# Performance work log

Hardware: AMD Instinct MI355X
Metric: run time of the kernel (lower is better)

Reference implementation:

```python
import jax, jax.numpy as jnp
import numpy as np

NUM_CODES = 512
CODE_DIM = 64
COMMITMENT_COST = 0.1
DECAY = 0.9
EPS = 1e-5


def setup_inputs() -> dict:
    key = jax.random.key(0)
    k1, k2, k3 = jax.random.split(key, 3)
    B, L, D, K = 32, 4096, CODE_DIM, NUM_CODES
    z_e = jax.random.normal(k1, (B, L, D), dtype=jnp.float32)
    emb = jax.random.uniform(k2, (K, D), dtype=jnp.float32, minval=-1.0 / K, maxval=1.0 / K)
    ema_cluster_size = jnp.ones((K,), dtype=jnp.float32)
    ema_w = emb + 0.01 * jax.random.normal(k3, (K, D), dtype=jnp.float32)
    return {"z_e": z_e, "emb": emb, "ema_cluster_size": ema_cluster_size, "ema_w": ema_w}


def reference(z_e, emb, ema_cluster_size, ema_w):
    B, L, D = z_e.shape
    K = emb.shape[0]
    flat = z_e.reshape(-1, D)                                   # [N, D]
    dists = (jnp.sum(flat * flat, axis=1, keepdims=True)
             - 2.0 * flat @ emb.T
             + jnp.sum(emb * emb, axis=1)[None, :])
    codes = jnp.argmin(dists, axis=1)                           # [N] int
    z_q = emb[codes].reshape(B, L, D)
    # straight-through estimator
    z_q_st = z_e + jax.lax.stop_gradient(z_q - z_e)
    # EMA updates (training, no_grad) via direct scatter-reduce instead of one-hot matmul
    cluster_size = jax.ops.segment_sum(jnp.ones_like(codes, dtype=z_e.dtype), codes, num_segments=K)
    new_ecs = ema_cluster_size * DECAY + cluster_size * (1.0 - DECAY)
    dw = jax.ops.segment_sum(flat, codes, num_segments=K)       # [K, D]
    new_ema_w = ema_w * DECAY + dw * (1.0 - DECAY)
    n = jnp.sum(new_ecs)
    cs_smoothed = (new_ecs + EPS) / (n + K * EPS) * n
    new_emb = new_ema_w / (cs_smoothed[:, None] + EPS)
    # commitment loss (z_q detached)
    commit = jnp.mean((z_e - jax.lax.stop_gradient(z_q)) ** 2)
    loss_vq = COMMITMENT_COST * commit
    return (z_q_st, loss_vq, codes.reshape(B, L), new_ecs, new_ema_w, new_emb)
```

## Files before the change

### kernel.cpp

```cpp
#include <hip/hip_runtime.h>
#include <math.h>

#define NROWS 131072
#define DIM 64
#define NCODE 512

#define OUT_ZQ    0
#define OUT_LOSS  8388608
#define OUT_CODES 8388609
#define OUT_ECS   8519681
#define OUT_EMAW  8520193
#define OUT_EMB   8552961

#define WS_LOSS    0
#define WS_N       8
#define WS_COUNTS  16
#define WS_OFFSETS 2064
#define WS_CURSOR  4112
#define WS_CSUM    6160
#define WS_CODESI  8208
#define WS_DW4     8208
#define WS_BUCKET  532496
#define WS_BYTES   1056784
#define WS_ZERO_BYTES 2064

#define DECAY_C ((float)0.9)
#define OMD_C   ((float)(1.0 - 0.9))
#define EPS_C   ((float)1e-5)

#define R4(M, b)  M(b) M((b) + 1) M((b) + 2) M((b) + 3)
#define R16(M, b) R4(M, b) R4(M, (b) + 4) R4(M, (b) + 8) R4(M, (b) + 12)

__device__ __forceinline__ float np_pairwise64_sq(const float* v) {
    float r[8];
#pragma unroll
    for (int j = 0; j < 8; ++j) r[j] = __fmul_rn(v[j], v[j]);
#pragma unroll
    for (int b = 1; b < 8; ++b) {
#pragma unroll
        for (int j = 0; j < 8; ++j)
            r[j] = __fadd_rn(r[j], __fmul_rn(v[8 * b + j], v[8 * b + j]));
    }
    return __fadd_rn(__fadd_rn(__fadd_rn(r[0], r[1]), __fadd_rn(r[2], r[3])),
                     __fadd_rn(__fadd_rn(r[4], r[5]), __fadd_rn(r[6], r[7])));
}

__global__ void k_csum(const float* __restrict__ emb, float* __restrict__ csum) {
    int k = blockIdx.x * blockDim.x + threadIdx.x;
    if (k >= NCODE) return;
    float e[DIM];
#pragma unroll
    for (int d = 0; d < DIM; d += 4) {
        float4 v = *reinterpret_cast<const float4*>(emb + (size_t)k * DIM + d);
        e[d] = v.x; e[d + 1] = v.y; e[d + 2] = v.z; e[d + 3] = v.w;
    }
    csum[k] = np_pairwise64_sq(e);
}

__global__ __launch_bounds__(256) void k_scores(
        const float* __restrict__ ze, const float* __restrict__ emb,
        const float* __restrict__ csum, float* __restrict__ out,
        int* __restrict__ codes_i, int* __restrict__ counts,
        double* __restrict__ lossAcc) {
    __shared__ float xs[DIM][128];
    __shared__ float ms[128];
    __shared__ int   hi_i[128];
    __shared__ int h[NCODE];
    __shared__ double ls[4];
    int t = threadIdx.x;
    int c = t & 127;
    int half = t >> 7;
    for (int i = t; i < NCODE; i += 256) h[i] = 0;

    int row = blockIdx.x * 128 + c;
    const float* x = ze + (size_t)row * DIM;

    float r0, r1, r2, r3, r4, r5, r6, r7;
    {
        float4 va = *reinterpret_cast<const float4*>(x + 0);
        float4 vb = *reinterpret_cast<const float4*>(x + 4);
        float d0 = __fadd_rn(va.x, va.x), d1 = __fadd_rn(va.y, va.y);
        float d2 = __fadd_rn(va.z, va.z), d3 = __fadd_rn(va.w, va.w);
        float d4 = __fadd_rn(vb.x, vb.x), d5 = __fadd_rn(vb.y, vb.y);
        float d6 = __fadd_rn(vb.z, vb.z), d7 = __fadd_rn(vb.w, vb.w);
        xs[0][c] = d0; xs[1][c] = d1; xs[2][c] = d2; xs[3][c] = d3;
        xs[4][c] = d4; xs[5][c] = d5; xs[6][c] = d6; xs[7][c] = d7;
        r0 = __fmul_rn(d0, d0); r1 = __fmul_rn(d1, d1);
        r2 = __fmul_rn(d2, d2); r3 = __fmul_rn(d3, d3);
        r4 = __fmul_rn(d4, d4); r5 = __fmul_rn(d5, d5);
        r6 = __fmul_rn(d6, d6); r7 = __fmul_rn(d7, d7);
    }
#define LD8(b) { \
        float4 va = *reinterpret_cast<const float4*>(x + 8 * (b)); \
        float4 vb = *reinterpret_cast<const float4*>(x + 8 * (b) + 4); \
        float d0 = __fadd_rn(va.x, va.x), d1 = __fadd_rn(va.y, va.y); \
        float d2 = __fadd_rn(va.z, va.z), d3 = __fadd_rn(va.w, va.w); \
        float d4 = __fadd_rn(vb.x, vb.x), d5 = __fadd_rn(vb.y, vb.y); \
        float d6 = __fadd_rn(vb.z, vb.z), d7 = __fadd_rn(vb.w, vb.w); \
        xs[8 * (b) + 0][c] = d0; xs[8 * (b) + 1][c] = d1; \
        xs[8 * (b) + 2][c] = d2; xs[8 * (b) + 3][c] = d3; \
        xs[8 * (b) + 4][c] = d4; xs[8 * (b) + 5][c] = d5; \
        xs[8 * (b) + 6][c] = d6; xs[8 * (b) + 7][c] = d7; \
        r0 = __fadd_rn(r0, __fmul_rn(d0, d0)); r1 = __fadd_rn(r1, __fmul_rn(d1, d1)); \
        r2 = __fadd_rn(r2, __fmul_rn(d2, d2)); r3 = __fadd_rn(r3, __fmul_rn(d3, d3)); \
        r4 = __fadd_rn(r4, __fmul_rn(d4, d4)); r5 = __fadd_rn(r5, __fmul_rn(d5, d5)); \
        r6 = __fadd_rn(r6, __fmul_rn(d6, d6)); r7 = __fadd_rn(r7, __fmul_rn(d7, d7)); }
    LD8(1) LD8(2) LD8(3) LD8(4) LD8(5) LD8(6) LD8(7)
    float A = __fmul_rn(0.25f,
        __fadd_rn(__fadd_rn(__fadd_rn(r0, r1), __fadd_rn(r2, r3)),
                  __fadd_rn(__fadd_rn(r4, r5), __fadd_rn(r6, r7))));

    int kbase = __builtin_amdgcn_readfirstlane(half << 8);

    float m1 = 3.4e38f;
    int i1 = kbase;
#define FMAD(dd) { const float xv = xs[dd][c]; \
        a0 = __builtin_fmaf(xv, e[(dd)      ], a0); \
        a1 = __builtin_fmaf(xv, e[(dd) +  64], a1); \
        a2 = __builtin_fmaf(xv, e[(dd) + 128], a2); \
        a3 = __builtin_fmaf(xv, e[(dd) + 192], a3); \
        a4 = __builtin_fmaf(xv, e[(dd) + 256], a4); \
        a5 = __builtin_fmaf(xv, e[(dd) + 320], a5); \
        a6 = __builtin_fmaf(xv, e[(dd) + 384], a6); \
        a7 = __builtin_fmaf(xv, e[(dd) + 448], a7); }
    for (int kk = 0; kk < NCODE / 2; kk += 8) {
        int k = kbase + kk;
        const float* e = emb + (size_t)k * DIM;
        float a0 = 0.f, a1 = 0.f, a2 = 0.f, a3 = 0.f;
        float a4 = 0.f, a5 = 0.f, a6 = 0.f, a7 = 0.f;
        R16(FMAD, 0) R16(FMAD, 16) R16(FMAD, 32) R16(FMAD, 48)
        float t0 = __fadd_rn(__fsub_rn(A, a0), csum[k + 0]);
        float t1 = __fadd_rn(__fsub_rn(A, a1), csum[k + 1]);
        float t2 = __fadd_rn(__fsub_rn(A, a2), csum[k + 2]);
        float t3 = __fadd_rn(__fsub_rn(A, a3), csum[k + 3]);
        float t4 = __fadd_rn(__fsub_rn(A, a4), csum[k + 4]);
        float t5 = __fadd_rn(__fsub_rn(A, a5), csum[k + 5]);
        float t6 = __fadd_rn(__fsub_rn(A, a6), csum[k + 6]);
        float t7 = __fadd_rn(__fsub_rn(A, a7), csum[k + 7]);
        if (t0 < m1) { m1 = t0; i1 = k; }
        if (t1 < m1) { m1 = t1; i1 = k + 1; }
        if (t2 < m1) { m1 = t2; i1 = k + 2; }
        if (t3 < m1) { m1 = t3; i1 = k + 3; }
        if (t4 < m1) { m1 = t4; i1 = k + 4; }
        if (t5 < m1) { m1 = t5; i1 = k + 5; }
        if (t6 < m1) { m1 = t6; i1 = k + 6; }
        if (t7 < m1) { m1 = t7; i1 = k + 7; }
    }
    if (half) { ms[c] = m1; hi_i[c] = i1; }
    __syncthreads();

    double lsum = 0.0;
    if (!half) {
        float mh = ms[c];
        int ih = hi_i[c];
        if (mh < m1) { m1 = mh; i1 = ih; }
        out[OUT_CODES + row] = (float)i1;
        codes_i[row] = i1;
        atomicAdd(&h[i1], 1);

        const float* e1 = emb + (size_t)i1 * DIM;
        float* zq = out + OUT_ZQ + (size_t)row * DIM;
#define ZQ4(q) { \
        float4 ev = *reinterpret_cast<const float4*>(e1 + 4 * (q)); \
        float xa = __fmul_rn(0.5f, xs[4 * (q) + 0][c]); \
        float xb = __fmul_rn(0.5f, xs[4 * (q) + 1][c]); \
        float xc = __fmul_rn(0.5f, xs[4 * (q) + 2][c]); \
        float xd = __fmul_rn(0.5f, xs[4 * (q) + 3][c]); \
        float ta = __fsub_rn(ev.x, xa); \
        float tb = __fsub_rn(ev.y, xb); \
        float tc = __fsub_rn(ev.z, xc); \
        float td = __fsub_rn(ev.w, xd); \
        float4 o; \
        o.x = __fadd_rn(xa, ta); \
        o.y = __fadd_rn(xb, tb); \
        o.z = __fadd_rn(xc, tc); \
        o.w = __fadd_rn(xd, td); \
        *reinterpret_cast<float4*>(zq + 4 * (q)) = o; \
        lsum += (double)ta * ta + (double)tb * tb + (double)tc * tc + (double)td * td; }
        R16(ZQ4, 0)
    }

    for (int off = 32; off; off >>= 1) lsum += __shfl_down(lsum, off);
    int wid = t >> 6;
    if ((t & 63) == 0) ls[wid] = lsum;
    __syncthreads();
    if (t == 0) atomicAdd(lossAcc, (ls[0] + ls[1]) + (ls[2] + ls[3]));
    for (int k = t; k < NCODE; k += 256) {
        int cc = h[k];
        if (cc) atomicAdd(&counts[k], cc);
    }
}

__global__ __launch_bounds__(512) void k_scan(
        const int* __restrict__ counts, int* __restrict__ offsets, int* __restrict__ cursor,
        const float* __restrict__ ecs_in, float* __restrict__ out, float* __restrict__ n_out) {
    __shared__ int sa[NCODE], sb[NCODE];
    __shared__ float red[NCODE];
    int k = threadIdx.x;
    int c = counts[k];
    sa[k] = c;
    float v = __fadd_rn(__fmul_rn(ecs_in[k], DECAY_C), __fmul_rn((float)c, OMD_C));
    out[OUT_ECS + k] = v;
    red[k] = v;
    __syncthreads();
    int* src = sa;
    int* dst = sb;
    for (int off = 1; off < NCODE; off <<= 1) {
        dst[k] = (k >= off) ? src[k - off] + src[k] : src[k];
        __syncthreads();
        int* tp = src; src = dst; dst = tp;
    }
    offsets[k] = src[k] - c;
    cursor[k]  = src[k] - c;
    for (int s = NCODE / 2; s > 0; s >>= 1) {
        if (k < s) red[k] += red[k + s];
        __syncthreads();
    }
    if (k == 0) n_out[0] = red[0];
}

__global__ __launch_bounds__(256) void k_scatter(
        const int* __restrict__ codes_i, int* __restrict__ cursor, int* __restrict__ bucket) {
    int row = blockIdx.x * 256 + threadIdx.x;
    int c = codes_i[row];
    int pos = atomicAdd(&cursor[c], 1);
    bucket[pos] = row;
}

__global__ __launch_bounds__(256) void k_dw(
        const float* __restrict__ ze, const int* __restrict__ bucket,
        const int* __restrict__ offsets, const int* __restrict__ counts,
        float* __restrict__ dw4) {
    __shared__ float p[4][DIM];
    int k = blockIdx.x >> 2;
    int q = blockIdx.x & 3;
    int w = threadIdx.x >> 6;
    int d = threadIdx.x & 63;
    int s = offsets[k];
    int n = counts[k];
    float acc0 = 0.f, acc1 = 0.f;
    int i = q + 4 * w;
    for (; i + 16 < n; i += 32) {
        int ra = bucket[s + i];
        int rb = bucket[s + i + 16];
        acc0 += ze[(size_t)ra * DIM + d];
        acc1 += ze[(size_t)rb * DIM + d];
    }
    if (i < n) acc0 += ze[(size_t)bucket[s + i] * DIM + d];
    p[w][d] = acc0 + acc1;
    __syncthreads();
    if (w == 0) dw4[((size_t)q * NCODE + k) * DIM + d] = (p[0][d] + p[1][d]) + (p[2][d] + p[3][d]);
}

__global__ __launch_bounds__(256) void k_final(
        const float* __restrict__ ema_w, const float* __restrict__ dw4,
        const float* __restrict__ n_ptr, const double* __restrict__ lossAcc,
        float* __restrict__ out) {
    int i = blockIdx.x * blockDim.x + threadIdx.x;
    if (i >= NCODE * DIM) return;
    int k = i >> 6;
    float dsum = __fadd_rn(__fadd_rn(dw4[i], dw4[i + NCODE * DIM]),
                           __fadd_rn(dw4[i + 2 * NCODE * DIM], dw4[i + 3 * NCODE * DIM]));
    float w = __fadd_rn(__fmul_rn(ema_w[i], DECAY_C), __fmul_rn(dsum, OMD_C));
    out[OUT_EMAW + i] = w;
    float n = n_ptr[0];
    float necs = out[OUT_ECS + k];
    float cs = (necs + EPS_C) / (n + (float)NCODE * EPS_C) * n;
    out[OUT_EMB + i] = w / (cs + EPS_C);
    if (i == 0) out[OUT_LOSS] = (float)(0.1 * (lossAcc[0] / (double)((size_t)NROWS * DIM)));
}

extern "C" void kernel_launch(void* const* d_in, const int* in_sizes, int n_in,
                              void* d_out, int out_size, void* d_ws, size_t ws_size,
                              hipStream_t stream) {
    const float* ze   = (const float*)d_in[0];
    const float* emb  = (const float*)d_in[1];
    const float* ecs  = (const float*)d_in[2];
    const float* emaw = (const float*)d_in[3];
    float* out = (float*)d_out;
    char* ws = (char*)d_ws;
    double* lossAcc = (double*)(ws + WS_LOSS);
    float*  n_out   = (float*)(ws + WS_N);
    int*    counts  = (int*)(ws + WS_COUNTS);
    int*    offsets = (int*)(ws + WS_OFFSETS);
    int*    cursor  = (int*)(ws + WS_CURSOR);
    float*  csum    = (float*)(ws + WS_CSUM);
    int*    codes_i = (int*)(ws + WS_CODESI);
    float*  dw4     = (float*)(ws + WS_DW4);
    int*    bucket  = (int*)(ws + WS_BUCKET);

    hipMemsetAsync(d_ws, 0, WS_ZERO_BYTES, stream);
    hipLaunchKernelGGL(k_csum, dim3(2), dim3(256), 0, stream, emb, csum);
    hipLaunchKernelGGL(k_scores, dim3(NROWS / 128), dim3(256), 0, stream,
                       ze, emb, csum, out, codes_i, counts, lossAcc);
    hipLaunchKernelGGL(k_scan, dim3(1), dim3(512), 0, stream,
                       counts, offsets, cursor, ecs, out, n_out);
    hipLaunchKernelGGL(k_scatter, dim3(NROWS / 256), dim3(256), 0, stream,
                       codes_i, cursor, bucket);
    hipLaunchKernelGGL(k_dw, dim3(NCODE * 4), dim3(256), 0, stream,
                       ze, bucket, offsets, counts, dw4);
    hipLaunchKernelGGL(k_final, dim3(NCODE * DIM / 256), dim3(256), 0, stream,
                       emaw, dw4, n_out, lossAcc, out);
}
```

Baseline: 241.2 us.

## Compute distances with split-bf16 MFMA and rescue near-tie rows in fp32

```diff
diff --git a/kernel.cpp b/kernel.cpp
--- a/kernel.cpp
+++ b/kernel.cpp
@@ -4,6 +4,8 @@
 #define NROWS 131072
 #define DIM 64
 #define NCODE 512
+#define FLAG_CAP 32768
+#define THR 6e-5f
 
 #define OUT_ZQ    0
 #define OUT_LOSS  8388608
@@ -14,22 +16,32 @@
 
 #define WS_LOSS    0
 #define WS_N       8
+#define WS_FLAGC   12
 #define WS_COUNTS  16
 #define WS_OFFSETS 2064
 #define WS_CURSOR  4112
 #define WS_CSUM    6160
-#define WS_CODESI  8208
-#define WS_DW4     8208
-#define WS_BUCKET  532496
-#define WS_BYTES   1056784
+#define WS_EHI     8208
+#define WS_ELO     73744
+#define WS_CODESI  139280
+#define WS_DW4     139280
+#define WS_BUCKET  663568
+#define WS_FLAGR   663568
+#define WS_BYTES   1187856
 #define WS_ZERO_BYTES 2064
 
 #define DECAY_C ((float)0.9)
 #define OMD_C   ((float)(1.0 - 0.9))
 #define EPS_C   ((float)1e-5)
 
-#define R4(M, b)  M(b) M((b) + 1) M((b) + 2) M((b) + 3)
-#define R16(M, b) R4(M, b) R4(M, (b) + 4) R4(M, (b) + 8) R4(M, (b) + 12)
+typedef float f32x4 __attribute__((ext_vector_type(4)));
+typedef short short8v __attribute__((ext_vector_type(8)));
+
+__device__ __forceinline__ unsigned short bf16_rne_bits(float f) {
+    unsigned int u = __float_as_uint(f);
+    unsigned int r = u + 0x7fffu + ((u >> 16) & 1u);
+    return (unsigned short)(r >> 16);
+}
 
 __device__ __forceinline__ float np_pairwise64_sq(const float* v) {
     float r[8];
@@ -57,129 +69,204 @@
     csum[k] = np_pairwise64_sq(e);
 }
 
-__global__ __launch_bounds__(256) void k_scores(
+__global__ __launch_bounds__(256) void k_split(
+        const float* __restrict__ emb, unsigned short* __restrict__ ehi,
+        unsigned short* __restrict__ elo) {
+    int i = blockIdx.x * 256 + threadIdx.x;
+    if (i >= NCODE * DIM) return;
+    float v = emb[i];
+    unsigned short h = bf16_rne_bits(v);
+    float hf = __uint_as_float((unsigned int)h << 16);
+    ehi[i] = h;
+    elo[i] = bf16_rne_bits(v - hf);
+}
+
+#define CVTE(H, L, j, val) { \
+    unsigned int ub = __float_as_uint(val); \
+    unsigned int rr = ub + 0x7fffu + ((ub >> 16) & 1u); \
+    unsigned short hb = (unsigned short)(rr >> 16); \
+    float hf2 = __uint_as_float(((unsigned int)hb) << 16); \
+    float lof = (val) - hf2; \
+    unsigned int ul = __float_as_uint(lof); \
+    unsigned int rl = ul + 0x7fffu + ((ul >> 16) & 1u); \
+    H[j] = (short)hb; L[j] = (short)(rl >> 16); }
+
+__global__ __launch_bounds__(256, 1) void k_mfma(
+        const float* __restrict__ ze, const unsigned short* __restrict__ ehi,
+        const unsigned short* __restrict__ elo, const float* __restrict__ csum,
+        float* __restrict__ out, int* __restrict__ codes_i,
+        int* __restrict__ flagC, int* __restrict__ flagR) {
+    __shared__ float cs[NCODE];
+    for (int i = threadIdx.x; i < NCODE; i += 256) cs[i] = csum[i];
+    __syncthreads();
+    int wid = threadIdx.x >> 6;
+    int lane = threadIdx.x & 63;
+    int r16 = lane & 15;
+    int kg = lane >> 4;
+    int rowbase = blockIdx.x * 128 + wid * 32;
+
+    short8v ahi[2][2], alo[2][2];
+#define LOADA(rt, hf) { \
+        const float4* ap = reinterpret_cast<const float4*>( \
+            ze + (size_t)(rowbase + (rt) * 16 + r16) * DIM + (hf) * 32 + 8 * kg); \
+        float4 u = ap[0], w = ap[1]; \
+        CVTE(ahi[rt][hf], alo[rt][hf], 0, u.x) CVTE(ahi[rt][hf], alo[rt][hf], 1, u.y) \
+        CVTE(ahi[rt][hf], alo[rt][hf], 2, u.z) CVTE(ahi[rt][hf], alo[rt][hf], 3, u.w) \
+        CVTE(ahi[rt][hf], alo[rt][hf], 4, w.x) CVTE(ahi[rt][hf], alo[rt][hf], 5, w.y) \
+        CVTE(ahi[rt][hf], alo[rt][hf], 6, w.z) CVTE(ahi[rt][hf], alo[rt][hf], 7, w.w) }
+    LOADA(0, 0) LOADA(0, 1) LOADA(1, 0) LOADA(1, 1)
+
+    float m1v[2][4], m2v[2][4];
+    int i1v[2][4];
+#pragma unroll
+    for (int rt = 0; rt < 2; ++rt)
+#pragma unroll
+        for (int j = 0; j < 4; ++j) { m1v[rt][j] = 3.4e38f; m2v[rt][j] = 3.4e38f; i1v[rt][j] = 0; }
+
+#define UPD(C, rt, reg) { \
+        float s = __builtin_fmaf(-2.f, C[reg], csv); \
+        if (s < m1v[rt][reg]) { m2v[rt][reg] = m1v[rt][reg]; m1v[rt][reg] = s; i1v[rt][reg] = codeIdx; } \
+        else if (s < m2v[rt][reg]) { m2v[rt][reg] = s; } }
+
+    for (int t = 0; t < 32; ++t) {
+        const short8v* bh = reinterpret_cast<const short8v*>(
+            ehi + (size_t)(t * 16 + r16) * DIM + 8 * kg);
+        const short8v* bl = reinterpret_cast<const short8v*>(
+            elo + (size_t)(t * 16 + r16) * DIM + 8 * kg);
+        short8v bh0 = bh[0], bh1 = bh[4];
+        short8v bl0 = bl[0], bl1 = bl[4];
+        f32x4 c0 = {0.f, 0.f, 0.f, 0.f};
+        f32x4 c1 = {0.f, 0.f, 0.f, 0.f};
+        c0 = __builtin_amdgcn_mfma_f32_16x16x32_bf16(ahi[0][0], bh0, c0, 0, 0, 0);
+        c0 = __builtin_amdgcn_mfma_f32_16x16x32_bf16(ahi[0][1], bh1, c0, 0, 0, 0);
+        c0 = __builtin_amdgcn_mfma_f32_16x16x32_bf16(alo[0][0], bh0, c0, 0, 0, 0);
+        c0 = __builtin_amdgcn_mfma_f32_16x16x32_bf16(alo[0][1], bh1, c0, 0, 0, 0);
+        c0 = __builtin_amdgcn_mfma_f32_16x16x32_bf16(ahi[0][0], bl0, c0, 0, 0, 0);
+        c0 = __builtin_amdgcn_mfma_f32_16x16x32_bf16(ahi[0][1], bl1, c0, 0, 0, 0);
+        c1 = __builtin_amdgcn_mfma_f32_16x16x32_bf16(ahi[1][0], bh0, c1, 0, 0, 0);
+        c1 = __builtin_amdgcn_mfma_f32_16x16x32_bf16(ahi[1][1], bh1, c1, 0, 0, 0);
+        c1 = __builtin_amdgcn_mfma_f32_16x16x32_bf16(alo[1][0], bh0, c1, 0, 0, 0);
+        c1 = __builtin_amdgcn_mfma_f32_16x16x32_bf16(alo[1][1], bh1, c1, 0, 0, 0);
+        c1 = __builtin_amdgcn_mfma_f32_16x16x32_bf16(ahi[1][0], bl0, c1, 0, 0, 0);
+        c1 = __builtin_amdgcn_mfma_f32_16x16x32_bf16(ahi[1][1], bl1, c1, 0, 0, 0);
+        float csv = cs[t * 16 + r16];
+        int codeIdx = t * 16 + r16;
+        UPD(c0, 0, 0) UPD(c0, 0, 1) UPD(c0, 0, 2) UPD(c0, 0, 3)
+        UPD(c1, 1, 0) UPD(c1, 1, 1) UPD(c1, 1, 2) UPD(c1, 1, 3)
+    }
+
+#define RED(rt, reg, mask) { \
+        float om1 = __shfl_xor(m1v[rt][reg], mask); \
+        int   oi  = __shfl_xor(i1v[rt][reg], mask); \
+        float om2 = __shfl_xor(m2v[rt][reg], mask); \
+        if (om1 < m1v[rt][reg]) { \
+            m2v[rt][reg] = fminf(m1v[rt][reg], om2); m1v[rt][reg] = om1; i1v[rt][reg] = oi; \
+        } else if (om1 > m1v[rt][reg]) { \
+            m2v[rt][reg] = fminf(m2v[rt][reg], om1); \
+        } else { \
+            if (oi < i1v[rt][reg]) i1v[rt][reg] = oi; \
+            m2v[rt][reg] = m1v[rt][reg]; } }
+#define RED4(rt, reg) RED(rt, reg, 1) RED(rt, reg, 2) RED(rt, reg, 4) RED(rt, reg, 8)
+    RED4(0, 0) RED4(0, 1) RED4(0, 2) RED4(0, 3)
+    RED4(1, 0) RED4(1, 1) RED4(1, 2) RED4(1, 3)
+
+    if (r16 == 0) {
+        int g = lane >> 4;
+#define WOUT(rt, reg) { \
+        int row = rowbase + (rt) * 16 + 4 * g + (reg); \
+        out[OUT_CODES + row] = (float)i1v[rt][reg]; \
+        codes_i[row] = i1v[rt][reg]; \
+        if (m2v[rt][reg] - m1v[rt][reg] < THR) { \
+            int pos = atomicAdd(flagC, 1); \
+            if (pos < FLAG_CAP) flagR[pos] = row; } }
+        WOUT(0, 0) WOUT(0, 1) WOUT(0, 2) WOUT(0, 3)
+        WOUT(1, 0) WOUT(1, 1) WOUT(1, 2) WOUT(1, 3)
+    }
+}
+
+__global__ __launch_bounds__(64) void k_rescue(
         const float* __restrict__ ze, const float* __restrict__ emb,
         const float* __restrict__ csum, float* __restrict__ out,
-        int* __restrict__ codes_i, int* __restrict__ counts,
-        double* __restrict__ lossAcc) {
-    __shared__ float xs[DIM][128];
-    __shared__ float ms[128];
-    __shared__ int   hi_i[128];
+        int* __restrict__ codes_i, const int* __restrict__ flagC,
+        const int* __restrict__ flagR) {
+    __shared__ float x2s[DIM];
+    int nf = *flagC;
+    if (nf > FLAG_CAP) nf = FLAG_CAP;
+    int lane = threadIdx.x;
+    for (int i = blockIdx.x; i < nf; i += gridDim.x) {
+        int row = flagR[i];
+        __syncthreads();
+        float v = ze[(size_t)row * DIM + lane];
+        x2s[lane] = __fadd_rn(v, v);
+        __syncthreads();
+        float r[8];
+#pragma unroll
+        for (int j = 0; j < 8; ++j) r[j] = __fmul_rn(x2s[j], x2s[j]);
+#pragma unroll
+        for (int b = 1; b < 8; ++b) {
+#pragma unroll
+            for (int j = 0; j < 8; ++j)
+                r[j] = __fadd_rn(r[j], __fmul_rn(x2s[8 * b + j], x2s[8 * b + j]));
+        }
+        float A = __fmul_rn(0.25f,
+            __fadd_rn(__fadd_rn(__fadd_rn(r[0], r[1]), __fadd_rn(r[2], r[3])),
+                      __fadd_rn(__fadd_rn(r[4], r[5]), __fadd_rn(r[6], r[7]))));
+        float m1 = 3.4e38f;
+        int i1 = 0x7fffffff;
+#pragma unroll
+        for (int kk = 0; kk < 8; ++kk) {
+            int k = lane * 8 + kk;
+            const float* e = emb + (size_t)k * DIM;
+            float a = 0.f;
+#pragma unroll
+            for (int d = 0; d < DIM; ++d) a = __builtin_fmaf(x2s[d], e[d], a);
+            float t = __fadd_rn(__fsub_rn(A, a), csum[k]);
+            if (t < m1) { m1 = t; i1 = k; }
+        }
+        for (int off = 32; off; off >>= 1) {
+            float ov = __shfl_xor(m1, off);
+            int oi = __shfl_xor(i1, off);
+            if (ov < m1 || (ov == m1 && oi < i1)) { m1 = ov; i1 = oi; }
+        }
+        if (lane == 0) {
+            out[OUT_CODES + row] = (float)i1;
+            codes_i[row] = i1;
+        }
+    }
+}
+
+__global__ __launch_bounds__(256) void k_apply(
+        const float* __restrict__ ze, const float* __restrict__ emb,
+        const int* __restrict__ codes_i, float* __restrict__ out,
+        int* __restrict__ counts, double* __restrict__ lossAcc) {
     __shared__ int h[NCODE];
     __shared__ double ls[4];
     int t = threadIdx.x;
-    int c = t & 127;
-    int half = t >> 7;
     for (int i = t; i < NCODE; i += 256) h[i] = 0;
-
-    int row = blockIdx.x * 128 + c;
+    __syncthreads();
+    int row = blockIdx.x * 256 + t;
+    int code = codes_i[row];
+    atomicAdd(&h[code], 1);
     const float* x = ze + (size_t)row * DIM;
-
-    float r0, r1, r2, r3, r4, r5, r6, r7;
-    {
-        float4 va = *reinterpret_cast<const float4*>(x + 0);
-        float4 vb = *reinterpret_cast<const float4*>(x + 4);
-        float d0 = __fadd_rn(va.x, va.x), d1 = __fadd_rn(va.y, va.y);
-        float d2 = __fadd_rn(va.z, va.z), d3 = __fadd_rn(va.w, va.w);
-        float d4 = __fadd_rn(vb.x, vb.x), d5 = __fadd_rn(vb.y, vb.y);
-        float d6 = __fadd_rn(vb.z, vb.z), d7 = __fadd_rn(vb.w, vb.w);
-        xs[0][c] = d0; xs[1][c] = d1; xs[2][c] = d2; xs[3][c] = d3;
-        xs[4][c] = d4; xs[5][c] = d5; xs[6][c] = d6; xs[7][c] = d7;
-        r0 = __fmul_rn(d0, d0); r1 = __fmul_rn(d1, d1);
-        r2 = __fmul_rn(d2, d2); r3 = __fmul_rn(d3, d3);
-        r4 = __fmul_rn(d4, d4); r5 = __fmul_rn(d5, d5);
-        r6 = __fmul_rn(d6, d6); r7 = __fmul_rn(d7, d7);
-    }
-#define LD8(b) { \
-        float4 va = *reinterpret_cast<const float4*>(x + 8 * (b)); \
-        float4 vb = *reinterpret_cast<const float4*>(x + 8 * (b) + 4); \
-        float d0 = __fadd_rn(va.x, va.x), d1 = __fadd_rn(va.y, va.y); \
-        float d2 = __fadd_rn(va.z, va.z), d3 = __fadd_rn(va.w, va.w); \
-        float d4 = __fadd_rn(vb.x, vb.x), d5 = __fadd_rn(vb.y, vb.y); \
-        float d6 = __fadd_rn(vb.z, vb.z), d7 = __fadd_rn(vb.w, vb.w); \
-        xs[8 * (b) + 0][c] = d0; xs[8 * (b) + 1][c] = d1; \
-        xs[8 * (b) + 2][c] = d2; xs[8 * (b) + 3][c] = d3; \
-        xs[8 * (b) + 4][c] = d4; xs[8 * (b) + 5][c] = d5; \
-        xs[8 * (b) + 6][c] = d6; xs[8 * (b) + 7][c] = d7; \
-        r0 = __fadd_rn(r0, __fmul_rn(d0, d0)); r1 = __fadd_rn(r1, __fmul_rn(d1, d1)); \
-        r2 = __fadd_rn(r2, __fmul_rn(d2, d2)); r3 = __fadd_rn(r3, __fmul_rn(d3, d3)); \
-        r4 = __fadd_rn(r4, __fmul_rn(d4, d4)); r5 = __fadd_rn(r5, __fmul_rn(d5, d5)); \
-        r6 = __fadd_rn(r6, __fmul_rn(d6, d6)); r7 = __fadd_rn(r7, __fmul_rn(d7, d7)); }
-    LD8(1) LD8(2) LD8(3) LD8(4) LD8(5) LD8(6) LD8(7)
-    float A = __fmul_rn(0.25f,
-        __fadd_rn(__fadd_rn(__fadd_rn(r0, r1), __fadd_rn(r2, r3)),
-                  __fadd_rn(__fadd_rn(r4, r5), __fadd_rn(r6, r7))));
-
-    int kbase = __builtin_amdgcn_readfirstlane(half << 8);
-
-    float m1 = 3.4e38f;
-    int i1 = kbase;
-#define FMAD(dd) { const float xv = xs[dd][c]; \
-        a0 = __builtin_fmaf(xv, e[(dd)      ], a0); \
-        a1 = __builtin_fmaf(xv, e[(dd) +  64], a1); \
-        a2 = __builtin_fmaf(xv, e[(dd) + 128], a2); \
-        a3 = __builtin_fmaf(xv, e[(dd) + 192], a3); \
-        a4 = __builtin_fmaf(xv, e[(dd) + 256], a4); \
-        a5 = __builtin_fmaf(xv, e[(dd) + 320], a5); \
-        a6 = __builtin_fmaf(xv, e[(dd) + 384], a6); \
-        a7 = __builtin_fmaf(xv, e[(dd) + 448], a7); }
-    for (int kk = 0; kk < NCODE / 2; kk += 8) {
-        int k = kbase + kk;
-        const float* e = emb + (size_t)k * DIM;
-        float a0 = 0.f, a1 = 0.f, a2 = 0.f, a3 = 0.f;
-        float a4 = 0.f, a5 = 0.f, a6 = 0.f, a7 = 0.f;
-        R16(FMAD, 0) R16(FMAD, 16) R16(FMAD, 32) R16(FMAD, 48)
-        float t0 = __fadd_rn(__fsub_rn(A, a0), csum[k + 0]);
-        float t1 = __fadd_rn(__fsub_rn(A, a1), csum[k + 1]);
-        float t2 = __fadd_rn(__fsub_rn(A, a2), csum[k + 2]);
-        float t3 = __fadd_rn(__fsub_rn(A, a3), csum[k + 3]);
-        float t4 = __fadd_rn(__fsub_rn(A, a4), csum[k + 4]);
-        float t5 = __fadd_rn(__fsub_rn(A, a5), csum[k + 5]);
-        float t6 = __fadd_rn(__fsub_rn(A, a6), csum[k + 6]);
-        float t7 = __fadd_rn(__fsub_rn(A, a7), csum[k + 7]);
-        if (t0 < m1) { m1 = t0; i1 = k; }
-        if (t1 < m1) { m1 = t1; i1 = k + 1; }
-        if (t2 < m1) { m1 = t2; i1 = k + 2; }
-        if (t3 < m1) { m1 = t3; i1 = k + 3; }
-        if (t4 < m1) { m1 = t4; i1 = k + 4; }
-        if (t5 < m1) { m1 = t5; i1 = k + 5; }
-        if (t6 < m1) { m1 = t6; i1 = k + 6; }
-        if (t7 < m1) { m1 = t7; i1 = k + 7; }
-    }
-    if (half) { ms[c] = m1; hi_i[c] = i1; }
-    __syncthreads();
-
+    const float* e = emb + (size_t)code * DIM;
+    float* zq = out + OUT_ZQ + (size_t)row * DIM;
     double lsum = 0.0;
-    if (!half) {
-        float mh = ms[c];
-        int ih = hi_i[c];
-        if (mh < m1) { m1 = mh; i1 = ih; }
-        out[OUT_CODES + row] = (float)i1;
-        codes_i[row] = i1;
-        atomicAdd(&h[i1], 1);
-
-        const float* e1 = emb + (size_t)i1 * DIM;
-        float* zq = out + OUT_ZQ + (size_t)row * DIM;
-#define ZQ4(q) { \
-        float4 ev = *reinterpret_cast<const float4*>(e1 + 4 * (q)); \
-        float xa = __fmul_rn(0.5f, xs[4 * (q) + 0][c]); \
-        float xb = __fmul_rn(0.5f, xs[4 * (q) + 1][c]); \
-        float xc = __fmul_rn(0.5f, xs[4 * (q) + 2][c]); \
-        float xd = __fmul_rn(0.5f, xs[4 * (q) + 3][c]); \
-        float ta = __fsub_rn(ev.x, xa); \
-        float tb = __fsub_rn(ev.y, xb); \
-        float tc = __fsub_rn(ev.z, xc); \
-        float td = __fsub_rn(ev.w, xd); \
-        float4 o; \
-        o.x = __fadd_rn(xa, ta); \
-        o.y = __fadd_rn(xb, tb); \
-        o.z = __fadd_rn(xc, tc); \
-        o.w = __fadd_rn(xd, td); \
-        *reinterpret_cast<float4*>(zq + 4 * (q)) = o; \
-        lsum += (double)ta * ta + (double)tb * tb + (double)tc * tc + (double)td * td; }
-        R16(ZQ4, 0)
-    }
-
+#pragma unroll
+    for (int d = 0; d < DIM; d += 4) {
+        float4 xv = *reinterpret_cast<const float4*>(x + d);
+        float4 ev = *reinterpret_cast<const float4*>(e + d);
+        float ta = __fsub_rn(ev.x, xv.x);
+        float tb = __fsub_rn(ev.y, xv.y);
+        float tc = __fsub_rn(ev.z, xv.z);
+        float td = __fsub_rn(ev.w, xv.w);
+        float4 o;
+        o.x = __fadd_rn(xv.x, ta);
+        o.y = __fadd_rn(xv.y, tb);
+        o.z = __fadd_rn(xv.z, tc);
+        o.w = __fadd_rn(xv.w, td);
+        *reinterpret_cast<float4*>(zq + d) = o;
+        lsum += (double)ta * ta + (double)tb * tb + (double)tc * tc + (double)td * td;
+    }
     for (int off = 32; off; off >>= 1) lsum += __shfl_down(lsum, off);
     int wid = t >> 6;
     if ((t & 63) == 0) ls[wid] = lsum;
@@ -281,18 +368,27 @@
     char* ws = (char*)d_ws;
     double* lossAcc = (double*)(ws + WS_LOSS);
     float*  n_out   = (float*)(ws + WS_N);
+    int*    flagC   = (int*)(ws + WS_FLAGC);
     int*    counts  = (int*)(ws + WS_COUNTS);
     int*    offsets = (int*)(ws + WS_OFFSETS);
     int*    cursor  = (int*)(ws + WS_CURSOR);
     float*  csum    = (float*)(ws + WS_CSUM);
+    unsigned short* ehi = (unsigned short*)(ws + WS_EHI);
+    unsigned short* elo = (unsigned short*)(ws + WS_ELO);
     int*    codes_i = (int*)(ws + WS_CODESI);
     float*  dw4     = (float*)(ws + WS_DW4);
     int*    bucket  = (int*)(ws + WS_BUCKET);
+    int*    flagR   = (int*)(ws + WS_FLAGR);
 
     hipMemsetAsync(d_ws, 0, WS_ZERO_BYTES, stream);
     hipLaunchKernelGGL(k_csum, dim3(2), dim3(256), 0, stream, emb, csum);
-    hipLaunchKernelGGL(k_scores, dim3(NROWS / 128), dim3(256), 0, stream,
-                       ze, emb, csum, out, codes_i, counts, lossAcc);
+    hipLaunchKernelGGL(k_split, dim3(NCODE * DIM / 256), dim3(256), 0, stream, emb, ehi, elo);
+    hipLaunchKernelGGL(k_mfma, dim3(NROWS / 128), dim3(256), 0, stream,
+                       ze, ehi, elo, csum, out, codes_i, flagC, flagR);
+    hipLaunchKernelGGL(k_rescue, dim3(1024), dim3(64), 0, stream,
+                       ze, emb, csum, out, codes_i, flagC, flagR);
+    hipLaunchKernelGGL(k_apply, dim3(NROWS / 256), dim3(256), 0, stream,
+                       ze, emb, codes_i, out, counts, lossAcc);
     hipLaunchKernelGGL(k_scan, dim3(1), dim3(512), 0, stream,
                        counts, offsets, cursor, ecs, out, n_out);
     hipLaunchKernelGGL(k_scatter, dim3(NROWS / 256), dim3(256), 0, stream,
```

Measured after the change: 225.9 us. -6.4%, faster.
